# Kernel optimization log

Measured on AMD Instinct MI355X. Metric: run time of the kernel, lower is better.

The kernel has to match this reference:

```python
import jax, jax.numpy as jnp
import numpy as np

EPS = 1e-8

def setup_inputs() -> dict:
    key = jax.random.key(0)
    k1, = jax.random.split(key, 1)
    B, C, T = 16, 256, 16000
    inp = jax.random.normal(k1, (B, C, T), dtype=jnp.float32)
    gain = jnp.ones((1, C, 1), dtype=jnp.float32)
    bias = jnp.zeros((1, C, 1), dtype=jnp.float32)
    return {"input": inp, "gain": gain, "bias": bias}

def reference(input, gain, bias):
    # input: [B, C, T]
    B, C, T = input.shape
    step_sum = input.sum(axis=1)            # [B, T]
    step_pow_sum = (input * input).sum(axis=1)  # [B, T]
    cum_sum = jnp.cumsum(step_sum, axis=1)      # [B, T]
    cum_pow_sum = jnp.cumsum(step_pow_sum, axis=1)
    # entry count: C, 2C, ..., T*C
    entry_cnt = (jnp.arange(1, T + 1, dtype=input.dtype) * C)[None, :]  # [1, T]
    cum_mean = cum_sum / entry_cnt
    cum_var = (cum_pow_sum - 2.0 * cum_mean * cum_sum) / entry_cnt + cum_mean * cum_mean
    cum_std = jnp.sqrt(cum_var + EPS)
    x = (input - cum_mean[:, None, :]) / cum_std[:, None, :]
    return x * gain + bias
```

## Files before the change

kernel.cpp:

```cpp
#include <hip/hip_runtime.h>

constexpr int B = 16;
constexpr int C = 256;
constexpr int T = 16000;
constexpr int Q = T / 4;
constexpr int SEG = 64;
constexpr int NSEG = (Q + SEG - 1) / SEG;
constexpr float EPS = 1e-8f;

typedef float f4 __attribute__((ext_vector_type(4)));

__global__ __launch_bounds__(256) void sumscan_kernel(
    const float* __restrict__ x,
    float* __restrict__ scan_s,
    float* __restrict__ scan_p,
    double* __restrict__ tot_s,
    double* __restrict__ tot_p) {
  const int seg = blockIdx.x;
  const int b   = blockIdx.y;
  const int w   = threadIdx.x >> 6;
  const int l   = threadIdx.x & 63;
  const int t4  = seg * SEG + l;
  const bool act = t4 < Q;

  f4 s = {0.f, 0.f, 0.f, 0.f};
  f4 p = {0.f, 0.f, 0.f, 0.f};
  if (act) {
    const f4* xb = reinterpret_cast<const f4*>(x + (size_t)b * C * T);
#pragma unroll 8
    for (int cc = 0; cc < C / 4; ++cc) {
      const int c = cc * 4 + w;
      f4 v = xb[(size_t)c * Q + t4];
      s += v;
      p += v * v;
    }
  }

  __shared__ f4 ls[4][64], lp[4][64];
  ls[w][l] = s;
  lp[w][l] = p;
  __syncthreads();

  if (w != 0) return;

  f4 cs = ls[0][l] + ls[1][l] + ls[2][l] + ls[3][l];
  f4 cp = lp[0][l] + lp[1][l] + lp[2][l] + lp[3][l];
  cs[1] += cs[0]; cs[2] += cs[1]; cs[3] += cs[2];
  cp[1] += cp[0]; cp[2] += cp[1]; cp[3] += cp[2];

  double rs = (double)cs[3], rp = (double)cp[3];
#pragma unroll
  for (int off = 1; off < 64; off <<= 1) {
    double ns = __shfl_up(rs, off);
    double np = __shfl_up(rp, off);
    if (l >= off) { rs += ns; rp += np; }
  }
  const double es = rs - (double)cs[3];
  const double ep = rp - (double)cp[3];

  if (act) {
    f4 os, op;
#pragma unroll
    for (int i = 0; i < 4; ++i) {
      os[i] = (float)(es + (double)cs[i]);
      op[i] = (float)(ep + (double)cp[i]);
    }
    reinterpret_cast<f4*>(scan_s + (size_t)b * T)[t4] = os;
    reinterpret_cast<f4*>(scan_p + (size_t)b * T)[t4] = op;
  }
  if (l == 63) {
    tot_s[b * NSEG + seg] = rs;
    tot_p[b * NSEG + seg] = rp;
  }
}

__global__ __launch_bounds__(256) void apply_kernel(
    const float* __restrict__ x,
    const float* __restrict__ scan_s,
    const float* __restrict__ scan_p,
    const double* __restrict__ tot_s,
    const double* __restrict__ tot_p,
    const float* __restrict__ gain,
    const float* __restrict__ bias,
    float* __restrict__ out) {
  const int seg = NSEG - 1 - blockIdx.x;
  const int b   = B - 1 - blockIdx.y;
  const int w   = threadIdx.x >> 6;
  const int l   = threadIdx.x & 63;
  const int t4  = seg * SEG + l;
  const bool act = t4 < Q;

  double vs = (l < seg) ? tot_s[b * NSEG + l] : 0.0;
  double vp = (l < seg) ? tot_p[b * NSEG + l] : 0.0;
#pragma unroll
  for (int off = 32; off > 0; off >>= 1) {
    vs += __shfl_xor(vs, off);
    vp += __shfl_xor(vp, off);
  }

  if (act) {
    const f4 cs = reinterpret_cast<const f4*>(scan_s + (size_t)b * T)[t4];
    const f4 cp = reinterpret_cast<const f4*>(scan_p + (size_t)b * T)[t4];
    f4 m, is;
#pragma unroll
    for (int i = 0; i < 4; ++i) {
      const int t = t4 * 4 + i;
      const float cnt  = (float)(t + 1) * (float)C;
      const float cums = (float)(vs + (double)cs[i]);
      const float cump = (float)(vp + (double)cp[i]);
      const float mean = cums / cnt;
      const float var  = cump / cnt - mean * mean;
      m[i]  = mean;
      is[i] = rsqrtf(var + EPS);
    }

    const f4* xb = reinterpret_cast<const f4*>(x   + (size_t)b * C * T);
    f4*       ob = reinterpret_cast<f4*>      (out + (size_t)b * C * T);
#pragma unroll 8
    for (int cc = 0; cc < C / 4; ++cc) {
      const int c = cc * 4 + w;
      const float g  = gain[c];
      const float bi = bias[c];
      f4 v = xb[(size_t)c * Q + t4];
      f4 o = (v - m) * is * g + bi;
      __builtin_nontemporal_store(o, &ob[(size_t)c * Q + t4]);
    }
  }
}

extern "C" void kernel_launch(void* const* d_in, const int* in_sizes, int n_in,
                              void* d_out, int out_size, void* d_ws, size_t ws_size,
                              hipStream_t stream) {
  const float* x    = (const float*)d_in[0];
  const float* gain = (const float*)d_in[1];
  const float* bias = (const float*)d_in[2];
  float* out = (float*)d_out;

  float*  scan_s = (float*)d_ws;
  float*  scan_p = scan_s + (size_t)B * T;
  double* tot_s  = (double*)(scan_p + (size_t)B * T);
  double* tot_p  = tot_s + (size_t)B * NSEG;

  dim3 grid(NSEG, B);
  sumscan_kernel<<<grid, 256, 0, stream>>>(x, scan_s, scan_p, tot_s, tot_p);
  apply_kernel<<<grid, 256, 0, stream>>>(x, scan_s, scan_p, tot_s, tot_p,
                                         gain, bias, out);
}
```

Measured before the change: 471.7 us.

## Fuse stats and normalize into single-pass decoupled-lookback scan kernel

Replaces the two-kernel approach (column sums plus scan, then a re-read of the input to normalize) with one kernel. Each block holds its input tile in registers and gets its prefix totals through a decoupled lookback over published per-segment aggregates, with ordering enforced by an atomic ticket. This avoids reading the input a second time from HBM and drops the intermediate scan arrays. In exchange it adds a flag-init kernel, spin-waiting on predecessor flags, and much higher register pressure from the 16 f4 values kept per thread, which may lower occupancy.

```diff
diff --git a/kernel.cpp b/kernel.cpp
--- a/kernel.cpp
+++ b/kernel.cpp
@@ -4,127 +4,162 @@
 constexpr int C = 256;
 constexpr int T = 16000;
 constexpr int Q = T / 4;
-constexpr int SEG = 64;
-constexpr int NSEG = (Q + SEG - 1) / SEG;
+constexpr int WSEG = 16;
+constexpr int NSEG = Q / WSEG;
 constexpr float EPS = 1e-8f;
+constexpr int NFLAG = B * NSEG;
 
 typedef float f4 __attribute__((ext_vector_type(4)));
 
-__global__ __launch_bounds__(256) void sumscan_kernel(
+#define SCOPE_AGENT __HIP_MEMORY_SCOPE_AGENT
+
+__device__ inline f4 shfl_xor_f4(f4 v, int m) {
+  f4 r;
+  r[0] = __shfl_xor(v[0], m); r[1] = __shfl_xor(v[1], m);
+  r[2] = __shfl_xor(v[2], m); r[3] = __shfl_xor(v[3], m);
+  return r;
+}
+
+__global__ __launch_bounds__(256) void init_flags(int* __restrict__ flags,
+                                                  int* __restrict__ ticket) {
+  const int i = blockIdx.x * 256 + threadIdx.x;
+  if (i < NFLAG) flags[i] = 0;
+  if (i == 0) *ticket = 0;
+}
+
+__global__ __launch_bounds__(256) void fused_kernel(
     const float* __restrict__ x,
-    float* __restrict__ scan_s,
-    float* __restrict__ scan_p,
-    double* __restrict__ tot_s,
-    double* __restrict__ tot_p) {
-  const int seg = blockIdx.x;
-  const int b   = blockIdx.y;
+    const float* __restrict__ gain,
+    const float* __restrict__ bias,
+    float* __restrict__ out,
+    int* __restrict__ flags,
+    int* __restrict__ ticket,
+    double* __restrict__ agg_s, double* __restrict__ agg_p,
+    double* __restrict__ inc_s, double* __restrict__ inc_p) {
+  __shared__ int vid_sh;
+  if (threadIdx.x == 0) vid_sh = atomicAdd(ticket, 1);
+  __syncthreads();
+  const int vid = vid_sh;
+  const int b   = vid / NSEG;
+  const int seg = vid - b * NSEG;
+
   const int w   = threadIdx.x >> 6;
   const int l   = threadIdx.x & 63;
-  const int t4  = seg * SEG + l;
-  const bool act = t4 < Q;
+  const int col = l & 15;
+  const int r   = l >> 4;
+  const int t4  = seg * WSEG + col;
+  const int fb  = b * NSEG;
 
-  f4 s = {0.f, 0.f, 0.f, 0.f};
-  f4 p = {0.f, 0.f, 0.f, 0.f};
-  if (act) {
-    const f4* xb = reinterpret_cast<const f4*>(x + (size_t)b * C * T);
-#pragma unroll 8
-    for (int cc = 0; cc < C / 4; ++cc) {
-      const int c = cc * 4 + w;
-      f4 v = xb[(size_t)c * Q + t4];
-      s += v;
-      p += v * v;
+  const f4* xb = reinterpret_cast<const f4*>(x + (size_t)b * C * T);
+  f4 v[16];
+  f4 s = {0.f, 0.f, 0.f, 0.f}, p = {0.f, 0.f, 0.f, 0.f};
+#pragma unroll
+  for (int k = 0; k < 16; ++k) {
+    const int c = r + 4 * w + 16 * k;
+    v[k] = __builtin_nontemporal_load(&xb[(size_t)c * Q + t4]);
+    s += v[k];
+    p += v[k] * v[k];
+  }
+  s += shfl_xor_f4(s, 16); p += shfl_xor_f4(p, 16);
+  s += shfl_xor_f4(s, 32); p += shfl_xor_f4(p, 32);
+
+  __shared__ f4 lss[4][16], lsp[4][16];
+  __shared__ f4 incl_s_l[16], incl_p_l[16];
+  __shared__ double excl_sh[2];
+  if (l < 16) { lss[w][col] = s; lsp[w][col] = p; }
+  __syncthreads();
+
+  if (w == 0) {
+    f4 cs = lss[0][col] + lss[1][col] + lss[2][col] + lss[3][col];
+    f4 cp = lsp[0][col] + lsp[1][col] + lsp[2][col] + lsp[3][col];
+    cs[1] += cs[0]; cs[2] += cs[1]; cs[3] += cs[2];
+    cp[1] += cp[0]; cp[2] += cp[1]; cp[3] += cp[2];
+    const float ts = cs[3], tp = cp[3];
+    float ps = ts, pp = tp;
+#pragma unroll
+    for (int off = 1; off < 16; off <<= 1) {
+      const float ns = __shfl_up(ps, off, 16);
+      const float np = __shfl_up(pp, off, 16);
+      if (col >= off) { ps += ns; pp += np; }
+    }
+    const float es = ps - ts, ep = pp - tp;
+    cs += es; cp += ep;
+    if (l < 16) { incl_s_l[col] = cs; incl_p_l[col] = cp; }
+    const double wtot_s = (double)__shfl(ps, 15, 16);
+    const double wtot_p = (double)__shfl(pp, 15, 16);
+
+    double ex_s = 0.0, ex_p = 0.0;
+    if (seg > 0) {
+      if (l == 0) {
+        __hip_atomic_store(&agg_s[fb + seg], wtot_s, __ATOMIC_RELAXED, SCOPE_AGENT);
+        __hip_atomic_store(&agg_p[fb + seg], wtot_p, __ATOMIC_RELAXED, SCOPE_AGENT);
+        __hip_atomic_store(&flags[fb + seg], 1, __ATOMIC_RELEASE, SCOPE_AGENT);
+      }
+      int base = seg - 1;
+      for (;;) {
+        const int idx = base - l;
+        int f;
+        for (;;) {
+          f = (idx >= 0) ? __hip_atomic_load(&flags[fb + idx], __ATOMIC_ACQUIRE,
+                                             SCOPE_AGENT)
+                         : 2;
+          if (__all(f != 0)) break;
+          __builtin_amdgcn_s_sleep(1);
+        }
+        const unsigned long long m2 = __ballot(f == 2);
+        const int j0 = m2 ? (__ffsll((long long)m2) - 1) : 64;
+        double c_s = 0.0, c_p = 0.0;
+        if (idx >= 0) {
+          if (l < j0) {
+            c_s = __hip_atomic_load(&agg_s[fb + idx], __ATOMIC_RELAXED, SCOPE_AGENT);
+            c_p = __hip_atomic_load(&agg_p[fb + idx], __ATOMIC_RELAXED, SCOPE_AGENT);
+          } else if (l == j0) {
+            c_s = __hip_atomic_load(&inc_s[fb + idx], __ATOMIC_RELAXED, SCOPE_AGENT);
+            c_p = __hip_atomic_load(&inc_p[fb + idx], __ATOMIC_RELAXED, SCOPE_AGENT);
+          }
+        }
+#pragma unroll
+        for (int off = 32; off > 0; off >>= 1) {
+          c_s += __shfl_xor(c_s, off);
+          c_p += __shfl_xor(c_p, off);
+        }
+        ex_s += c_s; ex_p += c_p;
+        if (m2) break;
+        base -= 64;
+        if (base < 0) break;
+      }
+    }
+    if (l == 0) {
+      __hip_atomic_store(&inc_s[fb + seg], ex_s + wtot_s, __ATOMIC_RELAXED, SCOPE_AGENT);
+      __hip_atomic_store(&inc_p[fb + seg], ex_p + wtot_p, __ATOMIC_RELAXED, SCOPE_AGENT);
+      __hip_atomic_store(&flags[fb + seg], 2, __ATOMIC_RELEASE, SCOPE_AGENT);
+      excl_sh[0] = ex_s; excl_sh[1] = ex_p;
     }
   }
-
-  __shared__ f4 ls[4][64], lp[4][64];
-  ls[w][l] = s;
-  lp[w][l] = p;
   __syncthreads();
 
-  if (w != 0) return;
-
-  f4 cs = ls[0][l] + ls[1][l] + ls[2][l] + ls[3][l];
-  f4 cp = lp[0][l] + lp[1][l] + lp[2][l] + lp[3][l];
-  cs[1] += cs[0]; cs[2] += cs[1]; cs[3] += cs[2];
-  cp[1] += cp[0]; cp[2] += cp[1]; cp[3] += cp[2];
-
-  double rs = (double)cs[3], rp = (double)cp[3];
+  const double exs = excl_sh[0];
+  const double exq = excl_sh[1];
+  const f4 ws = incl_s_l[col];
+  const f4 wp = incl_p_l[col];
+  f4 mm, ii;
 #pragma unroll
-  for (int off = 1; off < 64; off <<= 1) {
-    double ns = __shfl_up(rs, off);
-    double np = __shfl_up(rp, off);
-    if (l >= off) { rs += ns; rp += np; }
+  for (int i = 0; i < 4; ++i) {
+    const int t = t4 * 4 + i;
+    const float cnt  = (float)(t + 1) * (float)C;
+    const float cums = (float)(exs + (double)ws[i]);
+    const float cump = (float)(exq + (double)wp[i]);
+    const float mean = cums / cnt;
+    const float var  = cump / cnt - mean * mean;
+    mm[i] = mean;
+    ii[i] = rsqrtf(var + EPS);
   }
-  const double es = rs - (double)cs[3];
-  const double ep = rp - (double)cp[3];
-
-  if (act) {
-    f4 os, op;
+  f4* ob = reinterpret_cast<f4*>(out + (size_t)b * C * T);
 #pragma unroll
-    for (int i = 0; i < 4; ++i) {
-      os[i] = (float)(es + (double)cs[i]);
-      op[i] = (float)(ep + (double)cp[i]);
-    }
-    reinterpret_cast<f4*>(scan_s + (size_t)b * T)[t4] = os;
-    reinterpret_cast<f4*>(scan_p + (size_t)b * T)[t4] = op;
-  }
-  if (l == 63) {
-    tot_s[b * NSEG + seg] = rs;
-    tot_p[b * NSEG + seg] = rp;
-  }
-}
-
-__global__ __launch_bounds__(256) void apply_kernel(
-    const float* __restrict__ x,
-    const float* __restrict__ scan_s,
-    const float* __restrict__ scan_p,
-    const double* __restrict__ tot_s,
-    const double* __restrict__ tot_p,
-    const float* __restrict__ gain,
-    const float* __restrict__ bias,
-    float* __restrict__ out) {
-  const int seg = NSEG - 1 - blockIdx.x;
-  const int b   = B - 1 - blockIdx.y;
-  const int w   = threadIdx.x >> 6;
-  const int l   = threadIdx.x & 63;
-  const int t4  = seg * SEG + l;
-  const bool act = t4 < Q;
-
-  double vs = (l < seg) ? tot_s[b * NSEG + l] : 0.0;
-  double vp = (l < seg) ? tot_p[b * NSEG + l] : 0.0;
-#pragma unroll
-  for (int off = 32; off > 0; off >>= 1) {
-    vs += __shfl_xor(vs, off);
-    vp += __shfl_xor(vp, off);
-  }
-
-  if (act) {
-    const f4 cs = reinterpret_cast<const f4*>(scan_s + (size_t)b * T)[t4];
-    const f4 cp = reinterpret_cast<const f4*>(scan_p + (size_t)b * T)[t4];
-    f4 m, is;
-#pragma unroll
-    for (int i = 0; i < 4; ++i) {
-      const int t = t4 * 4 + i;
-      const float cnt  = (float)(t + 1) * (float)C;
-      const float cums = (float)(vs + (double)cs[i]);
-      const float cump = (float)(vp + (double)cp[i]);
-      const float mean = cums / cnt;
-      const float var  = cump / cnt - mean * mean;
-      m[i]  = mean;
-      is[i] = rsqrtf(var + EPS);
-    }
-
-    const f4* xb = reinterpret_cast<const f4*>(x   + (size_t)b * C * T);
-    f4*       ob = reinterpret_cast<f4*>      (out + (size_t)b * C * T);
-#pragma unroll 8
-    for (int cc = 0; cc < C / 4; ++cc) {
-      const int c = cc * 4 + w;
-      const float g  = gain[c];
-      const float bi = bias[c];
-      f4 v = xb[(size_t)c * Q + t4];
-      f4 o = (v - m) * is * g + bi;
-      __builtin_nontemporal_store(o, &ob[(size_t)c * Q + t4]);
-    }
+  for (int k = 0; k < 16; ++k) {
+    const int c = r + 4 * w + 16 * k;
+    const f4 o = (v[k] - mm) * ii * gain[c] + bias[c];
+    __builtin_nontemporal_store(o, &ob[(size_t)c * Q + t4]);
   }
 }
 
@@ -136,13 +171,15 @@
   const float* bias = (const float*)d_in[2];
   float* out = (float*)d_out;
 
-  float*  scan_s = (float*)d_ws;
-  float*  scan_p = scan_s + (size_t)B * T;
-  double* tot_s  = (double*)(scan_p + (size_t)B * T);
-  double* tot_p  = tot_s + (size_t)B * NSEG;
+  double* agg_s = (double*)d_ws;
+  double* agg_p = agg_s + NFLAG;
+  double* inc_s = agg_p + NFLAG;
+  double* inc_p = inc_s + NFLAG;
+  int*    flags = (int*)(inc_p + NFLAG);
+  int*    ticket = flags + NFLAG;
 
-  dim3 grid(NSEG, B);
-  sumscan_kernel<<<grid, 256, 0, stream>>>(x, scan_s, scan_p, tot_s, tot_p);
-  apply_kernel<<<grid, 256, 0, stream>>>(x, scan_s, scan_p, tot_s, tot_p,
-                                         gain, bias, out);
+  init_flags<<<(NFLAG + 255) / 256, 256, 0, stream>>>(flags, ticket);
+
+  fused_kernel<<<NFLAG, 256, 0, stream>>>(x, gain, bias, out, flags, ticket,
+                                          agg_s, agg_p, inc_s, inc_p);
 }
```

After: 851.9 us. 80.6% more time.
